# Optimization experiments

Hardware: AMD Instinct MI355X
Metric: run time of the kernel (lower is better)

The kernel has to match this reference:

```python
import jax, jax.numpy as jnp
import numpy as np

N_NODES, N_EDGES, IN_DIM, H, D = 50000, 800000, 256, 4, 32
NEG_SLOPE = 0.2  # DGL GATv2Conv default


def setup_inputs() -> dict:
    key = jax.random.key(0)
    k = jax.random.split(key, 7)
    s_in = 1.0 / np.sqrt(IN_DIM)
    return {
        "h": jax.random.normal(k[0], (N_NODES, IN_DIM), jnp.float32),
        "src": jax.random.randint(k[1], (N_EDGES,), 0, N_NODES, jnp.int32),
        "dst": jax.random.randint(k[2], (N_EDGES,), 0, N_NODES, jnp.int32),
        "W_src": jax.random.normal(k[3], (IN_DIM, H * D), jnp.float32) * s_in,
        "b_src": jnp.zeros((H * D,), jnp.float32),
        "W_dst": jax.random.normal(k[4], (IN_DIM, H * D), jnp.float32) * s_in,
        "b_dst": jnp.zeros((H * D,), jnp.float32),
        "attn_a": jax.random.normal(k[5], (H, D), jnp.float32) * 0.1,
    }


def reference(h, src, dst, W_src, b_src, W_dst, b_dst, attn_a):
    """GATv2Conv (hop=1, get_attention=True) + reshape, as in TweetEmbedder.forward."""
    N = h.shape[0]
    el = (h @ W_src + b_src).reshape(N, H, D)  # fc_src, per-head
    er = (h @ W_dst + b_dst).reshape(N, H, D)  # fc_dst, per-head
    # edge scores: e_ij = a^T leaky_relu(W_src h_i + W_dst h_j)
    e = jax.nn.leaky_relu(el[src] + er[dst], NEG_SLOPE)          # (E, H, D)
    scores = jnp.einsum('ehd,hd->eh', e, attn_a)                  # (E, H)
    # edge softmax over incoming edges of each dst node
    m = jax.ops.segment_max(scores, dst, num_segments=N)          # (N, H)
    ex = jnp.exp(scores - m[dst])
    denom = jax.ops.segment_sum(ex, dst, num_segments=N)          # (N, H)
    a = ex / denom[dst]                                           # (E, H)
    # weighted scatter-aggregate of source messages
    out = jax.ops.segment_sum(a[:, :, None] * el[src], dst, num_segments=N)  # (N, H, D)
    return out.reshape(N, H * D), a[:, :, None]
```

## Files before the change

### kernel.cpp

```cpp
#include <hip/hip_runtime.h>
#include <cstdint>
#include <cstddef>

#define NNODES 50000
#define NEDGES 800000
#define INDIM  256
#define HD     128
#define NH     4
#define NEG    0.2f

#define SCAN_B ((NNODES + 255) / 256)

#define CONVH_BLKS (NNODES * INDIM / 8 / 256)
#define HIST_BLKS  ((NEDGES + 255) / 256)
#define CONVW_BLKS 64
#define GEMM_BLKS  (2 * ((NNODES + 127) / 128))
#define SCAT_BLKS  ((NEDGES + 255) / 256)

typedef __attribute__((ext_vector_type(8))) short   short8;
typedef __attribute__((ext_vector_type(8))) ushort  ushort8;
typedef __attribute__((ext_vector_type(4))) float   floatx4;

__device__ __forceinline__ ushort f2bf(float f) {
    unsigned u = __float_as_uint(f);
    unsigned r = u + 0x7fffu + ((u >> 16) & 1u);
    return (ushort)(r >> 16);
}
__device__ __forceinline__ float bf2f(ushort u) {
    return __uint_as_float(((unsigned)u) << 16);
}

__device__ __forceinline__ int swz(int c) { return c ^ ((c >> 4) & 7); }

__global__ __launch_bounds__(256) void fusedA_kernel(
        const float* __restrict__ h, ushort* __restrict__ h_bf,
        const int* __restrict__ dst, int* __restrict__ cnt_work,
        const float* __restrict__ Wsrc, const float* __restrict__ Wdst,
        ushort* __restrict__ Wt) {
    __shared__ float t[32][33];
    const int bid = blockIdx.x;
    const int tid = threadIdx.x;

    if (bid < CONVH_BLKS) {
        int idx = bid * 256 + tid;
        const int total = NNODES * INDIM / 8;
        if (idx >= total) return;
        const float* p = h + (size_t)idx * 8;
        float4 v0 = *(const float4*)p;
        float4 v1 = *(const float4*)(p + 4);
        ushort8 o;
        o[0] = f2bf(v0.x); o[1] = f2bf(v0.y); o[2] = f2bf(v0.z); o[3] = f2bf(v0.w);
        o[4] = f2bf(v1.x); o[5] = f2bf(v1.y); o[6] = f2bf(v1.z); o[7] = f2bf(v1.w);
        *(ushort8*)(h_bf + (size_t)idx * 8) = o;
    } else if (bid < CONVH_BLKS + HIST_BLKS) {
        int e = (bid - CONVH_BLKS) * 256 + tid;
        if (e < NEDGES) atomicAdd(cnt_work + dst[e], 1);
    } else {
        int wb = bid - (CONVH_BLKS + HIST_BLKS);
        int kb = (wb & 7) * 32, nb = (wb >> 3) * 32;
        int tx = tid & 31, ty = tid >> 5;
        for (int i = ty; i < 32; i += 8) {
            int k = kb + i, n = nb + tx;
            float v = (n < HD) ? Wsrc[(size_t)k * HD + n] : Wdst[(size_t)k * HD + (n - HD)];
            t[i][tx] = v;
        }
        __syncthreads();
        for (int i = ty; i < 32; i += 8) {
            int n = nb + i, k = kb + tx;
            Wt[(size_t)n * INDIM + k] = f2bf(t[tx][i]);
        }
    }
}

__global__ __launch_bounds__(256) void scan_partial_kernel(
        const int* __restrict__ cnt, int* __restrict__ partials) {
    __shared__ int lds[256];
    int i = blockIdx.x * 256 + threadIdx.x;
    lds[threadIdx.x] = (i < NNODES) ? cnt[i] : 0;
    __syncthreads();
    for (int off = 128; off > 0; off >>= 1) {
        if (threadIdx.x < off) lds[threadIdx.x] += lds[threadIdx.x + off];
        __syncthreads();
    }
    if (threadIdx.x == 0) partials[blockIdx.x] = lds[0];
}

__global__ __launch_bounds__(256) void scan_offsets_kernel(
        int* __restrict__ partials, int* __restrict__ rowptr) {
    __shared__ int lds[256];
    int t = threadIdx.x;
    int v = (t < SCAN_B) ? partials[t] : 0;
    lds[t] = v;
    __syncthreads();
    for (int off = 1; off < 256; off <<= 1) {
        int u = (t >= off) ? lds[t - off] : 0;
        __syncthreads();
        lds[t] += u;
        __syncthreads();
    }
    if (t < SCAN_B) partials[t] = lds[t] - v;
    if (t == 255) rowptr[NNODES] = lds[255];
}

__global__ __launch_bounds__(256) void scan_final_kernel(
        int* __restrict__ cnt_work, const int* __restrict__ partials,
        int* __restrict__ rowptr) {
    __shared__ int lds[256];
    int i = blockIdx.x * 256 + threadIdx.x;
    int t = threadIdx.x;
    int v = (i < NNODES) ? cnt_work[i] : 0;
    lds[t] = v;
    __syncthreads();
    for (int off = 1; off < 256; off <<= 1) {
        int u = (t >= off) ? lds[t - off] : 0;
        __syncthreads();
        lds[t] += u;
        __syncthreads();
    }
    if (i < NNODES) {
        int start = partials[blockIdx.x] + lds[t] - v;
        rowptr[i] = start;
        cnt_work[i] = start;
    }
}

__global__ __launch_bounds__(256) void fusedB_kernel(
        const ushort* __restrict__ h_bf, const ushort* __restrict__ Wt,
        const float* __restrict__ bsrc, const float* __restrict__ bdst,
        ushort* __restrict__ el_bf, float* __restrict__ er,
        const int* __restrict__ src, const int* __restrict__ dst,
        int* __restrict__ cnt_work,
        int* __restrict__ eidx, int* __restrict__ esrc) {
    __shared__ ushort As[512 * 8];
    __shared__ ushort Bs[512 * 8];

    const int bid = blockIdx.x;
    const int tid = threadIdx.x;

    if (bid >= GEMM_BLKS) {
        int e = (bid - GEMM_BLKS) * 256 + tid;
        if (e >= NEDGES) return;
        int s = src[e];
        int pos = atomicAdd(cnt_work + dst[e], 1);
        eidx[pos] = e;
        esrc[pos] = s;
        return;
    }

    const int bx = bid & 1, by = bid >> 1;
    const int wave = tid >> 6, lane = tid & 63;
    const int row0 = by * 128;
    const int col0 = bx * 128;
    const int l15  = lane & 15, quad = lane >> 4;

    floatx4 acc[2][8];
#pragma unroll
    for (int i = 0; i < 2; ++i)
#pragma unroll
        for (int j = 0; j < 8; ++j) acc[i][j] = (floatx4){0.f, 0.f, 0.f, 0.f};

    for (int kk = 0; kk < INDIM; kk += 32) {
#pragma unroll
        for (int it = 0; it < 2; ++it) {
            int idx = tid + it * 256;
            int r = idx >> 2;
            int kq = idx & 3;
            int c = (r >> 4) * 64 + kq * 16 + (r & 15);
            int grow = row0 + r;
            ushort8 aw = (ushort8){0,0,0,0,0,0,0,0};
            if (grow < NNODES)
                aw = *(const ushort8*)(h_bf + (size_t)grow * INDIM + kk + kq * 8);
            *(ushort8*)(As + swz(c) * 8) = aw;
            ushort8 bw = *(const ushort8*)(Wt + (size_t)(col0 + r) * INDIM + kk + kq * 8);
            *(ushort8*)(Bs + swz(c) * 8) = bw;
        }
        __syncthreads();

        short8 af[2], bf[8];
#pragma unroll
        for (int tm = 0; tm < 2; ++tm) {
            int c = (wave * 2 + tm) * 64 + quad * 16 + l15;
            af[tm] = *(const short8*)(As + swz(c) * 8);
        }
#pragma unroll
        for (int tn = 0; tn < 8; ++tn) {
            int c = tn * 64 + quad * 16 + l15;
            bf[tn] = *(const short8*)(Bs + swz(c) * 8);
        }
#pragma unroll
        for (int tm = 0; tm < 2; ++tm)
#pragma unroll
            for (int tn = 0; tn < 8; ++tn)
                acc[tm][tn] = __builtin_amdgcn_mfma_f32_16x16x32_bf16(
                    af[tm], bf[tn], acc[tm][tn], 0, 0, 0);
        __syncthreads();
    }

    if (col0 == 0) {
#pragma unroll
        for (int tn = 0; tn < 8; ++tn) {
            int col = tn * 16 + l15;
            float bias = bsrc[col];
#pragma unroll
            for (int tm = 0; tm < 2; ++tm)
#pragma unroll
                for (int reg = 0; reg < 4; ++reg) {
                    int row = row0 + wave * 32 + tm * 16 + quad * 4 + reg;
                    if (row < NNODES)
                        el_bf[(size_t)row * HD + col] = f2bf(acc[tm][tn][reg] + bias);
                }
        }
    } else {
#pragma unroll
        for (int tn = 0; tn < 8; ++tn) {
            int col = tn * 16 + l15;
            float bias = bdst[col];
#pragma unroll
            for (int tm = 0; tm < 2; ++tm)
#pragma unroll
                for (int reg = 0; reg < 4; ++reg) {
                    int row = row0 + wave * 32 + tm * 16 + quad * 4 + reg;
                    if (row < NNODES)
                        er[(size_t)row * HD + col] = acc[tm][tn][reg] + bias;
                }
        }
    }
}

#define DEGCAP 128

__global__ __launch_bounds__(256) void node_fused_kernel(
        const ushort* __restrict__ el_bf, const float* __restrict__ er,
        const int* __restrict__ rowptr, const int* __restrict__ eidx,
        const int* __restrict__ esrc,
        const float* __restrict__ attn,
        float* __restrict__ out_feat, float* __restrict__ out_a) {
    __shared__ float sp[4][DEGCAP * NH];

    const int wv = threadIdx.x >> 6;
    const int n = blockIdx.x * 4 + wv;
    if (n >= NNODES) return;
    const int lane = threadIdx.x & 63;
    const int hh = lane >> 4;
    const int lo = rowptr[n], hi = rowptr[n + 1];
    const int deg = hi - lo;
    float* spw = sp[wv];
    const int l2 = lane * 2;

    const float2 rv = *(const float2*)(er + (size_t)n * HD + l2);
    const float a0 = attn[l2], a1 = attn[l2 + 1];

    float m = -3.4e38f, lsum = 0.0f, acc0 = 0.0f, acc1 = 0.0f;

    if (deg > 0 && deg <= DEGCAP) {
        int jj0 = (lane & 15);
        if (jj0 >= deg) jj0 = deg - 1;
        int si = esrc[lo + jj0];

        for (int base = 0; base < deg; base += 16) {
            ushort2 u[16];
#pragma unroll
            for (int j = 0; j < 16; ++j) {
                if (base + j < deg) {
                    int s = __builtin_amdgcn_readlane(si, j);
                    u[j] = *(const ushort2*)(el_bf + (size_t)s * HD + l2);
                }
            }
            int si_nxt = si;
            if (base + 16 < deg) {
                int jj = base + 16 + (lane & 15);
                if (jj >= deg) jj = deg - 1;
                si_nxt = esrc[lo + jj];
            }
#pragma unroll
            for (int j = 0; j < 16; ++j) {
                if (base + j < deg) {
                    float evx = bf2f(u[j].x), evy = bf2f(u[j].y);
                    float x0 = evx + rv.x; x0 = x0 > 0.f ? x0 : NEG * x0;
                    float x1 = evy + rv.y; x1 = x1 > 0.f ? x1 : NEG * x1;
                    float p = x0 * a0 + x1 * a1;
                    p += __shfl_xor(p, 1, 16);
                    p += __shfl_xor(p, 2, 16);
                    p += __shfl_xor(p, 4, 16);
                    p += __shfl_xor(p, 8, 16);
                    if ((lane & 15) == 0) spw[(base + j) * NH + hh] = p;
                    float mn = fmaxf(m, p);
                    float sc = __expf(m - mn);
                    float w  = __expf(p - mn);
                    lsum = lsum * sc + w;
                    acc0 = acc0 * sc + w * evx;
                    acc1 = acc1 * sc + w * evy;
                    m = mn;
                }
            }
            si = si_nxt;
        }
    } else if (deg > DEGCAP) {
        ushort2 u = {0,0};
        { int s_ = esrc[lo]; u = *(const ushort2*)(el_bf + (size_t)s_ * HD + l2); }
        for (int i = lo; i < hi; ++i) {
            float evx = bf2f(u.x), evy = bf2f(u.y);
            if (i + 1 < hi) { int s_ = esrc[i + 1];
                u = *(const ushort2*)(el_bf + (size_t)s_ * HD + l2); }
            float x0 = evx + rv.x; x0 = x0 > 0.f ? x0 : NEG * x0;
            float x1 = evy + rv.y; x1 = x1 > 0.f ? x1 : NEG * x1;
            float p = x0 * a0 + x1 * a1;
            p += __shfl_xor(p, 1, 16);
            p += __shfl_xor(p, 2, 16);
            p += __shfl_xor(p, 4, 16);
            p += __shfl_xor(p, 8, 16);
            float mn = fmaxf(m, p);
            float sc = __expf(m - mn);
            float w  = __expf(p - mn);
            lsum = lsum * sc + w;
            acc0 = acc0 * sc + w * evx;
            acc1 = acc1 * sc + w * evy;
            m = mn;
        }
    }

    float2 o;
    if (deg == 0) { o.x = 0.0f; o.y = 0.0f; }
    else { float inv = 1.0f / lsum; o.x = acc0 * inv; o.y = acc1 * inv; }
    *(float2*)(out_feat + (size_t)n * HD + l2) = o;

    if (deg == 0) return;

    float inv = 1.0f / lsum;
    if (deg <= DEGCAP) {
        float mh   = __shfl(m,   (lane & 3) << 4, 64);
        float invh = __shfl(inv, (lane & 3) << 4, 64);
        for (int j = (lane >> 2); j < deg; j += 16) {
            int e = eidx[lo + j];
            float p = spw[j * NH + (lane & 3)];
            out_a[(size_t)e * NH + (lane & 3)] = __expf(p - mh) * invh;
        }
    } else {
        for (int i = lo; i < hi; ++i) {
            int s_ = esrc[i];
            ushort2 u = *(const ushort2*)(el_bf + (size_t)s_ * HD + l2);
            float evx = bf2f(u.x), evy = bf2f(u.y);
            float x0 = evx + rv.x; x0 = x0 > 0.f ? x0 : NEG * x0;
            float x1 = evy + rv.y; x1 = x1 > 0.f ? x1 : NEG * x1;
            float p = x0 * a0 + x1 * a1;
            p += __shfl_xor(p, 1, 16);
            p += __shfl_xor(p, 2, 16);
            p += __shfl_xor(p, 4, 16);
            p += __shfl_xor(p, 8, 16);
            if ((lane & 15) == 0) {
                int e = eidx[i];
                out_a[(size_t)e * NH + hh] = __expf(p - m) * inv;
            }
        }
    }
}

extern "C" void kernel_launch(void* const* d_in, const int* in_sizes, int n_in,
                              void* d_out, int out_size, void* d_ws, size_t ws_size,
                              hipStream_t stream) {
    const float* h    = (const float*)d_in[0];
    const int*   src  = (const int*)d_in[1];
    const int*   dst  = (const int*)d_in[2];
    const float* Wsrc = (const float*)d_in[3];
    const float* bsrc = (const float*)d_in[4];
    const float* Wdst = (const float*)d_in[5];
    const float* bdst = (const float*)d_in[6];
    const float* attn = (const float*)d_in[7];

    float* out_feat = (float*)d_out;
    float* out_a    = out_feat + (size_t)NNODES * HD;

    ushort* h_bf = (ushort*)d_out;

    float*  er       = (float*)d_ws;
    ushort* Wt       = (ushort*)(er + (size_t)NNODES * HD);
    ushort* el_bf    = Wt + 2 * HD * INDIM;
    int*    cnt_work = (int*)(el_bf + (size_t)NNODES * HD);
    int*    eidx     = cnt_work + NNODES;
    int*    esrc     = eidx + NEDGES;
    int*    rowptr   = esrc + NEDGES;
    int*    partials = rowptr + NNODES + 1;

    hipMemsetAsync(cnt_work, 0, NNODES * sizeof(int), stream);

    fusedA_kernel<<<CONVH_BLKS + HIST_BLKS + CONVW_BLKS, 256, 0, stream>>>(
        h, h_bf, dst, cnt_work, Wsrc, Wdst, Wt);

    scan_partial_kernel<<<SCAN_B, 256, 0, stream>>>(cnt_work, partials);
    scan_offsets_kernel<<<1, 256, 0, stream>>>(partials, rowptr);
    scan_final_kernel<<<SCAN_B, 256, 0, stream>>>(cnt_work, partials, rowptr);

    fusedB_kernel<<<GEMM_BLKS + SCAT_BLKS, 256, 0, stream>>>(
        h_bf, Wt, bsrc, bdst, el_bf, er, src, dst, cnt_work, eidx, esrc);

    node_fused_kernel<<<(NNODES + 3) / 4, 256, 0, stream>>>(
        el_bf, er, rowptr, eidx, esrc, attn, out_feat, out_a);
}
```

Baseline: 270.8 us.

## Process eight edges per wave with 16-wide feature slices and interleaved edge pairs

Reworks the node aggregation kernel so each wave handles 8 incoming edges at once, with each lane owning a 16-element feature slice of one edge. Loads become 32-byte vector loads instead of 4-byte ones, with one-step prefetch of the next edge batch. Partial accumulators are merged across the 8 edge lanes with a butterfly transpose-reduce at the end. Edge index and source are packed into one int2 array so the scatter writes and the node-kernel reads are paired. The cost is higher register pressure from the 16-wide accumulators plus extra shuffles, and wasted lanes for nodes with small degree.

```diff
diff --git a/kernel.cpp b/kernel.cpp
--- a/kernel.cpp
+++ b/kernel.cpp
@@ -129,8 +129,7 @@
         const float* __restrict__ bsrc, const float* __restrict__ bdst,
         ushort* __restrict__ el_bf, float* __restrict__ er,
         const int* __restrict__ src, const int* __restrict__ dst,
-        int* __restrict__ cnt_work,
-        int* __restrict__ eidx, int* __restrict__ esrc) {
+        int* __restrict__ cnt_work, int2* __restrict__ epair) {
     __shared__ ushort As[512 * 8];
     __shared__ ushort Bs[512 * 8];
 
@@ -142,8 +141,7 @@
         if (e >= NEDGES) return;
         int s = src[e];
         int pos = atomicAdd(cnt_work + dst[e], 1);
-        eidx[pos] = e;
-        esrc[pos] = s;
+        epair[pos] = make_int2(e, s);
         return;
     }
 
@@ -231,8 +229,7 @@
 
 __global__ __launch_bounds__(256) void node_fused_kernel(
         const ushort* __restrict__ el_bf, const float* __restrict__ er,
-        const int* __restrict__ rowptr, const int* __restrict__ eidx,
-        const int* __restrict__ esrc,
+        const int* __restrict__ rowptr, const int2* __restrict__ epair,
         const float* __restrict__ attn,
         float* __restrict__ out_feat, float* __restrict__ out_a) {
     __shared__ float sp[4][DEGCAP * NH];
@@ -241,69 +238,158 @@
     const int n = blockIdx.x * 4 + wv;
     if (n >= NNODES) return;
     const int lane = threadIdx.x & 63;
-    const int hh = lane >> 4;
+    const int hh   = lane >> 4;
+    const int j8   = lane & 7;
+    const int dbase = (lane >> 3) * 16;
     const int lo = rowptr[n], hi = rowptr[n + 1];
     const int deg = hi - lo;
     float* spw = sp[wv];
-    const int l2 = lane * 2;
-
-    const float2 rv = *(const float2*)(er + (size_t)n * HD + l2);
-    const float a0 = attn[l2], a1 = attn[l2 + 1];
-
-    float m = -3.4e38f, lsum = 0.0f, acc0 = 0.0f, acc1 = 0.0f;
-
-    if (deg > 0 && deg <= DEGCAP) {
-        int jj0 = (lane & 15);
-        if (jj0 >= deg) jj0 = deg - 1;
-        int si = esrc[lo + jj0];
-
-        for (int base = 0; base < deg; base += 16) {
-            ushort2 u[16];
-#pragma unroll
-            for (int j = 0; j < 16; ++j) {
-                if (base + j < deg) {
-                    int s = __builtin_amdgcn_readlane(si, j);
-                    u[j] = *(const ushort2*)(el_bf + (size_t)s * HD + l2);
+
+    if (deg == 0) {
+        int o = (j8 & 1) * 8 + ((j8 >> 1) & 1) * 4 + ((j8 >> 2) & 1) * 2;
+        *(float2*)(out_feat + (size_t)n * HD + dbase + o) = make_float2(0.f, 0.f);
+        return;
+    }
+
+    if (deg <= DEGCAP) {
+        float erv[16], av[16], acc[16];
+        {
+            const float4* p4 = (const float4*)(er + (size_t)n * HD + dbase);
+            const float4* a4 = (const float4*)(attn + dbase);
+#pragma unroll
+            for (int q = 0; q < 4; ++q) {
+                float4 t = p4[q];
+                erv[4*q] = t.x; erv[4*q+1] = t.y; erv[4*q+2] = t.z; erv[4*q+3] = t.w;
+                float4 u = a4[q];
+                av[4*q] = u.x; av[4*q+1] = u.y; av[4*q+2] = u.z; av[4*q+3] = u.w;
+            }
+        }
+#pragma unroll
+        for (int d = 0; d < 16; ++d) acc[d] = 0.f;
+        float m = -3.4e38f, lsum = 0.f;
+
+        int t0 = (j8 < deg) ? j8 : (deg - 1);
+        int s_cur = epair[lo + t0].y;
+        uint4 el_lo, el_hi;
+        {
+            const ushort* ep = el_bf + (size_t)s_cur * HD + dbase;
+            el_lo = *(const uint4*)ep;
+            el_hi = *(const uint4*)(ep + 8);
+        }
+        int s_nxt = s_cur;
+        if (deg > 8) {
+            int t = 8 + j8; if (t >= deg) t = deg - 1;
+            s_nxt = epair[lo + t].y;
+        }
+
+        for (int base = 0; base < deg; base += 8) {
+            uint4 nl_lo = el_lo, nl_hi = el_hi;
+            if (base + 8 < deg) {
+                const ushort* ep = el_bf + (size_t)s_nxt * HD + dbase;
+                nl_lo = *(const uint4*)ep;
+                nl_hi = *(const uint4*)(ep + 8);
+            }
+            int s_n2 = s_nxt;
+            if (base + 16 < deg) {
+                int t = base + 16 + j8; if (t >= deg) t = deg - 1;
+                s_n2 = epair[lo + t].y;
+            }
+
+            float ev[16];
+            {
+                const unsigned* wl = (const unsigned*)&el_lo;
+                const unsigned* wh = (const unsigned*)&el_hi;
+#pragma unroll
+                for (int q = 0; q < 4; ++q) {
+                    ev[2*q]       = __uint_as_float(wl[q] << 16);
+                    ev[2*q + 1]   = __uint_as_float(wl[q] & 0xffff0000u);
+                    ev[8 + 2*q]   = __uint_as_float(wh[q] << 16);
+                    ev[8 + 2*q+1] = __uint_as_float(wh[q] & 0xffff0000u);
                 }
             }
-            int si_nxt = si;
-            if (base + 16 < deg) {
-                int jj = base + 16 + (lane & 15);
-                if (jj >= deg) jj = deg - 1;
-                si_nxt = esrc[lo + jj];
-            }
-#pragma unroll
-            for (int j = 0; j < 16; ++j) {
-                if (base + j < deg) {
-                    float evx = bf2f(u[j].x), evy = bf2f(u[j].y);
-                    float x0 = evx + rv.x; x0 = x0 > 0.f ? x0 : NEG * x0;
-                    float x1 = evy + rv.y; x1 = x1 > 0.f ? x1 : NEG * x1;
-                    float p = x0 * a0 + x1 * a1;
-                    p += __shfl_xor(p, 1, 16);
-                    p += __shfl_xor(p, 2, 16);
-                    p += __shfl_xor(p, 4, 16);
-                    p += __shfl_xor(p, 8, 16);
-                    if ((lane & 15) == 0) spw[(base + j) * NH + hh] = p;
-                    float mn = fmaxf(m, p);
-                    float sc = __expf(m - mn);
-                    float w  = __expf(p - mn);
-                    lsum = lsum * sc + w;
-                    acc0 = acc0 * sc + w * evx;
-                    acc1 = acc1 * sc + w * evy;
-                    m = mn;
-                }
-            }
-            si = si_nxt;
-        }
-    } else if (deg > DEGCAP) {
-        ushort2 u = {0,0};
-        { int s_ = esrc[lo]; u = *(const ushort2*)(el_bf + (size_t)s_ * HD + l2); }
+            float pa = 0.f, pb = 0.f;
+#pragma unroll
+            for (int d = 0; d < 16; d += 2) {
+                float x0 = ev[d]   + erv[d];   x0 = fmaxf(x0, NEG * x0);
+                float x1 = ev[d+1] + erv[d+1]; x1 = fmaxf(x1, NEG * x1);
+                pa = fmaf(x0, av[d],   pa);
+                pb = fmaf(x1, av[d+1], pb);
+            }
+            float part = pa + pb;
+            float p = part + __shfl_xor(part, 8, 64);
+            bool valid = (base + j8) < deg;
+            if (!valid) p = -3.4e38f;
+            if (valid && (lane & 8) == 0) spw[(base + j8) * NH + hh] = p;
+
+            float cm = p;
+            cm = fmaxf(cm, __shfl_xor(cm, 1, 64));
+            cm = fmaxf(cm, __shfl_xor(cm, 2, 64));
+            cm = fmaxf(cm, __shfl_xor(cm, 4, 64));
+            float mn = fmaxf(m, cm);
+            float sc = __expf(m - mn);
+            float w  = __expf(p - mn);
+            float ws = w;
+            ws += __shfl_xor(ws, 1, 64);
+            ws += __shfl_xor(ws, 2, 64);
+            ws += __shfl_xor(ws, 4, 64);
+            lsum = lsum * sc + ws;
+#pragma unroll
+            for (int d = 0; d < 16; ++d)
+                acc[d] = fmaf(w, ev[d], acc[d] * sc);
+            m = mn;
+            el_lo = nl_lo; el_hi = nl_hi; s_nxt = s_n2;
+        }
+
+        float inv = 1.0f / lsum;
+
+#pragma unroll
+        for (int k = 0; k < 8; ++k) {
+            float send = (j8 & 1) ? acc[k] : acc[k + 8];
+            float recv = __shfl_xor(send, 1, 64);
+            float keep = (j8 & 1) ? acc[k + 8] : acc[k];
+            acc[k] = keep + recv;
+        }
+#pragma unroll
+        for (int k = 0; k < 4; ++k) {
+            float send = (j8 & 2) ? acc[k] : acc[k + 4];
+            float recv = __shfl_xor(send, 2, 64);
+            float keep = (j8 & 2) ? acc[k + 4] : acc[k];
+            acc[k] = keep + recv;
+        }
+#pragma unroll
+        for (int k = 0; k < 2; ++k) {
+            float send = (j8 & 4) ? acc[k] : acc[k + 2];
+            float recv = __shfl_xor(send, 4, 64);
+            float keep = (j8 & 4) ? acc[k + 2] : acc[k];
+            acc[k] = keep + recv;
+        }
+        int o = (j8 & 1) * 8 + ((j8 >> 1) & 1) * 4 + ((j8 >> 2) & 1) * 2;
+        *(float2*)(out_feat + (size_t)n * HD + dbase + o) =
+            make_float2(acc[0] * inv, acc[1] * inv);
+
+        float mh   = __shfl(m,   (lane & 3) << 4, 64);
+        float invh = __shfl(inv, (lane & 3) << 4, 64);
+        for (int q = lane >> 2; q < deg; q += 16) {
+            int e = epair[lo + q].x;
+            float pq = spw[q * NH + (lane & 3)];
+            out_a[(size_t)e * NH + (lane & 3)] = __expf(pq - mh) * invh;
+        }
+        return;
+    }
+
+    {
+        const int l2 = lane * 2;
+        const float2 rv = *(const float2*)(er + (size_t)n * HD + l2);
+        const float a0 = attn[l2], a1 = attn[l2 + 1];
+        float m = -3.4e38f, lsum = 0.f, acc0 = 0.f, acc1 = 0.f;
+        ushort2 u;
+        { int s_ = epair[lo].y; u = *(const ushort2*)(el_bf + (size_t)s_ * HD + l2); }
         for (int i = lo; i < hi; ++i) {
             float evx = bf2f(u.x), evy = bf2f(u.y);
-            if (i + 1 < hi) { int s_ = esrc[i + 1];
+            if (i + 1 < hi) { int s_ = epair[i + 1].y;
                 u = *(const ushort2*)(el_bf + (size_t)s_ * HD + l2); }
-            float x0 = evx + rv.x; x0 = x0 > 0.f ? x0 : NEG * x0;
-            float x1 = evy + rv.y; x1 = x1 > 0.f ? x1 : NEG * x1;
+            float x0 = evx + rv.x; x0 = fmaxf(x0, NEG * x0);
+            float x1 = evy + rv.y; x1 = fmaxf(x1, NEG * x1);
             float p = x0 * a0 + x1 * a1;
             p += __shfl_xor(p, 1, 16);
             p += __shfl_xor(p, 2, 16);
@@ -317,38 +403,21 @@
             acc1 = acc1 * sc + w * evy;
             m = mn;
         }
-    }
-
-    float2 o;
-    if (deg == 0) { o.x = 0.0f; o.y = 0.0f; }
-    else { float inv = 1.0f / lsum; o.x = acc0 * inv; o.y = acc1 * inv; }
-    *(float2*)(out_feat + (size_t)n * HD + l2) = o;
-
-    if (deg == 0) return;
-
-    float inv = 1.0f / lsum;
-    if (deg <= DEGCAP) {
-        float mh   = __shfl(m,   (lane & 3) << 4, 64);
-        float invh = __shfl(inv, (lane & 3) << 4, 64);
-        for (int j = (lane >> 2); j < deg; j += 16) {
-            int e = eidx[lo + j];
-            float p = spw[j * NH + (lane & 3)];
-            out_a[(size_t)e * NH + (lane & 3)] = __expf(p - mh) * invh;
-        }
-    } else {
+        float inv = 1.0f / lsum;
+        *(float2*)(out_feat + (size_t)n * HD + l2) = make_float2(acc0 * inv, acc1 * inv);
         for (int i = lo; i < hi; ++i) {
-            int s_ = esrc[i];
-            ushort2 u = *(const ushort2*)(el_bf + (size_t)s_ * HD + l2);
-            float evx = bf2f(u.x), evy = bf2f(u.y);
-            float x0 = evx + rv.x; x0 = x0 > 0.f ? x0 : NEG * x0;
-            float x1 = evy + rv.y; x1 = x1 > 0.f ? x1 : NEG * x1;
+            int s_ = epair[i].y;
+            ushort2 uu = *(const ushort2*)(el_bf + (size_t)s_ * HD + l2);
+            float evx = bf2f(uu.x), evy = bf2f(uu.y);
+            float x0 = evx + rv.x; x0 = fmaxf(x0, NEG * x0);
+            float x1 = evy + rv.y; x1 = fmaxf(x1, NEG * x1);
             float p = x0 * a0 + x1 * a1;
             p += __shfl_xor(p, 1, 16);
             p += __shfl_xor(p, 2, 16);
             p += __shfl_xor(p, 4, 16);
             p += __shfl_xor(p, 8, 16);
             if ((lane & 15) == 0) {
-                int e = eidx[i];
+                int e = epair[i].x;
                 out_a[(size_t)e * NH + hh] = __expf(p - m) * inv;
             }
         }
@@ -376,9 +445,8 @@
     ushort* Wt       = (ushort*)(er + (size_t)NNODES * HD);
     ushort* el_bf    = Wt + 2 * HD * INDIM;
     int*    cnt_work = (int*)(el_bf + (size_t)NNODES * HD);
-    int*    eidx     = cnt_work + NNODES;
-    int*    esrc     = eidx + NEDGES;
-    int*    rowptr   = esrc + NEDGES;
+    int2*   epair    = (int2*)(cnt_work + NNODES);
+    int*    rowptr   = (int*)(epair + NEDGES);
     int*    partials = rowptr + NNODES + 1;
 
     hipMemsetAsync(cnt_work, 0, NNODES * sizeof(int), stream);
@@ -391,8 +459,8 @@
     scan_final_kernel<<<SCAN_B, 256, 0, stream>>>(cnt_work, partials, rowptr);
 
     fusedB_kernel<<<GEMM_BLKS + SCAT_BLKS, 256, 0, stream>>>(
-        h_bf, Wt, bsrc, bdst, el_bf, er, src, dst, cnt_work, eidx, esrc);
+        h_bf, Wt, bsrc, bdst, el_bf, er, src, dst, cnt_work, epair);
 
     node_fused_kernel<<<(NNODES + 3) / 4, 256, 0, stream>>>(
-        el_bf, er, rowptr, eidx, esrc, attn, out_feat, out_a);
-}
+        el_bf, er, rowptr, epair, attn, out_feat, out_a);
+}
```

Measured after the change: 311.5 us. +15.0%, slower.

## Fuse h bf16 conversion into GEMM, compute el and er per block, pack edge pairs

Applied to the files above, without the earlier changes.

Drops the separate h-to-bf16 conversion pass and converts fp32 h inside the GEMM tile load. Each GEMM block now computes all 256 output columns (el and er together), so h is read once instead of twice, at the cost of twice the accumulator registers and LDS for B. Edge index and source arrays are packed into one int2 array. The node kernel's online softmax is batched in groups of four edges to cut exp calls and shorten dependency chains.

```diff
diff --git a/kernel.cpp b/kernel.cpp
--- a/kernel.cpp
+++ b/kernel.cpp
@@ -11,10 +11,9 @@
 
 #define SCAN_B ((NNODES + 255) / 256)
 
-#define CONVH_BLKS (NNODES * INDIM / 8 / 256)
 #define HIST_BLKS  ((NEDGES + 255) / 256)
 #define CONVW_BLKS 64
-#define GEMM_BLKS  (2 * ((NNODES + 127) / 128))
+#define GEMM_BLKS  ((NNODES + 127) / 128)
 #define SCAT_BLKS  ((NEDGES + 255) / 256)
 
 typedef __attribute__((ext_vector_type(8))) short   short8;
@@ -33,7 +32,6 @@
 __device__ __forceinline__ int swz(int c) { return c ^ ((c >> 4) & 7); }
 
 __global__ __launch_bounds__(256) void fusedA_kernel(
-        const float* __restrict__ h, ushort* __restrict__ h_bf,
         const int* __restrict__ dst, int* __restrict__ cnt_work,
         const float* __restrict__ Wsrc, const float* __restrict__ Wdst,
         ushort* __restrict__ Wt) {
@@ -41,22 +39,11 @@
     const int bid = blockIdx.x;
     const int tid = threadIdx.x;
 
-    if (bid < CONVH_BLKS) {
-        int idx = bid * 256 + tid;
-        const int total = NNODES * INDIM / 8;
-        if (idx >= total) return;
-        const float* p = h + (size_t)idx * 8;
-        float4 v0 = *(const float4*)p;
-        float4 v1 = *(const float4*)(p + 4);
-        ushort8 o;
-        o[0] = f2bf(v0.x); o[1] = f2bf(v0.y); o[2] = f2bf(v0.z); o[3] = f2bf(v0.w);
-        o[4] = f2bf(v1.x); o[5] = f2bf(v1.y); o[6] = f2bf(v1.z); o[7] = f2bf(v1.w);
-        *(ushort8*)(h_bf + (size_t)idx * 8) = o;
-    } else if (bid < CONVH_BLKS + HIST_BLKS) {
-        int e = (bid - CONVH_BLKS) * 256 + tid;
+    if (bid < HIST_BLKS) {
+        int e = bid * 256 + tid;
         if (e < NEDGES) atomicAdd(cnt_work + dst[e], 1);
     } else {
-        int wb = bid - (CONVH_BLKS + HIST_BLKS);
+        int wb = bid - HIST_BLKS;
         int kb = (wb & 7) * 32, nb = (wb >> 3) * 32;
         int tx = tid & 31, ty = tid >> 5;
         for (int i = ty; i < 32; i += 8) {
@@ -124,15 +111,14 @@
     }
 }
 
-__global__ __launch_bounds__(256) void fusedB_kernel(
-        const ushort* __restrict__ h_bf, const ushort* __restrict__ Wt,
+__global__ __launch_bounds__(256, 2) void fusedB_kernel(
+        const float* __restrict__ h, const ushort* __restrict__ Wt,
         const float* __restrict__ bsrc, const float* __restrict__ bdst,
         ushort* __restrict__ el_bf, float* __restrict__ er,
         const int* __restrict__ src, const int* __restrict__ dst,
-        int* __restrict__ cnt_work,
-        int* __restrict__ eidx, int* __restrict__ esrc) {
+        int* __restrict__ cnt_work, int2* __restrict__ epair) {
     __shared__ ushort As[512 * 8];
-    __shared__ ushort Bs[512 * 8];
+    __shared__ ushort Bs[1024 * 8];
 
     const int bid = blockIdx.x;
     const int tid = threadIdx.x;
@@ -142,22 +128,19 @@
         if (e >= NEDGES) return;
         int s = src[e];
         int pos = atomicAdd(cnt_work + dst[e], 1);
-        eidx[pos] = e;
-        esrc[pos] = s;
+        epair[pos] = make_int2(e, s);
         return;
     }
 
-    const int bx = bid & 1, by = bid >> 1;
     const int wave = tid >> 6, lane = tid & 63;
-    const int row0 = by * 128;
-    const int col0 = bx * 128;
+    const int row0 = bid * 128;
     const int l15  = lane & 15, quad = lane >> 4;
 
-    floatx4 acc[2][8];
+    floatx4 acc[2][16];
 #pragma unroll
     for (int i = 0; i < 2; ++i)
 #pragma unroll
-        for (int j = 0; j < 8; ++j) acc[i][j] = (floatx4){0.f, 0.f, 0.f, 0.f};
+        for (int j = 0; j < 16; ++j) acc[i][j] = (floatx4){0.f, 0.f, 0.f, 0.f};
 
     for (int kk = 0; kk < INDIM; kk += 32) {
 #pragma unroll
@@ -168,62 +151,67 @@
             int c = (r >> 4) * 64 + kq * 16 + (r & 15);
             int grow = row0 + r;
             ushort8 aw = (ushort8){0,0,0,0,0,0,0,0};
-            if (grow < NNODES)
-                aw = *(const ushort8*)(h_bf + (size_t)grow * INDIM + kk + kq * 8);
+            if (grow < NNODES) {
+                const float* p = h + (size_t)grow * INDIM + kk + kq * 8;
+                float4 v0 = *(const float4*)p;
+                float4 v1 = *(const float4*)(p + 4);
+                aw[0] = f2bf(v0.x); aw[1] = f2bf(v0.y); aw[2] = f2bf(v0.z); aw[3] = f2bf(v0.w);
+                aw[4] = f2bf(v1.x); aw[5] = f2bf(v1.y); aw[6] = f2bf(v1.z); aw[7] = f2bf(v1.w);
+            }
             *(ushort8*)(As + swz(c) * 8) = aw;
-            ushort8 bw = *(const ushort8*)(Wt + (size_t)(col0 + r) * INDIM + kk + kq * 8);
+        }
+#pragma unroll
+        for (int it = 0; it < 4; ++it) {
+            int idx = tid + it * 256;
+            int r = idx >> 2;
+            int kq = idx & 3;
+            int c = (r >> 4) * 64 + kq * 16 + (r & 15);
+            ushort8 bw = *(const ushort8*)(Wt + (size_t)r * INDIM + kk + kq * 8);
             *(ushort8*)(Bs + swz(c) * 8) = bw;
         }
         __syncthreads();
 
-        short8 af[2], bf[8];
+        short8 af[2];
 #pragma unroll
         for (int tm = 0; tm < 2; ++tm) {
             int c = (wave * 2 + tm) * 64 + quad * 16 + l15;
             af[tm] = *(const short8*)(As + swz(c) * 8);
         }
 #pragma unroll
-        for (int tn = 0; tn < 8; ++tn) {
+        for (int tn = 0; tn < 16; ++tn) {
             int c = tn * 64 + quad * 16 + l15;
-            bf[tn] = *(const short8*)(Bs + swz(c) * 8);
-        }
+            short8 bfr = *(const short8*)(Bs + swz(c) * 8);
+            acc[0][tn] = __builtin_amdgcn_mfma_f32_16x16x32_bf16(af[0], bfr, acc[0][tn], 0, 0, 0);
+            acc[1][tn] = __builtin_amdgcn_mfma_f32_16x16x32_bf16(af[1], bfr, acc[1][tn], 0, 0, 0);
+        }
+        __syncthreads();
+    }
+
+#pragma unroll
+    for (int tn = 0; tn < 8; ++tn) {
+        int col = tn * 16 + l15;
+        float bias = bsrc[col];
 #pragma unroll
         for (int tm = 0; tm < 2; ++tm)
 #pragma unroll
-            for (int tn = 0; tn < 8; ++tn)
-                acc[tm][tn] = __builtin_amdgcn_mfma_f32_16x16x32_bf16(
-                    af[tm], bf[tn], acc[tm][tn], 0, 0, 0);
-        __syncthreads();
-    }
-
-    if (col0 == 0) {
-#pragma unroll
-        for (int tn = 0; tn < 8; ++tn) {
-            int col = tn * 16 + l15;
-            float bias = bsrc[col];
-#pragma unroll
-            for (int tm = 0; tm < 2; ++tm)
-#pragma unroll
-                for (int reg = 0; reg < 4; ++reg) {
-                    int row = row0 + wave * 32 + tm * 16 + quad * 4 + reg;
-                    if (row < NNODES)
-                        el_bf[(size_t)row * HD + col] = f2bf(acc[tm][tn][reg] + bias);
-                }
-        }
-    } else {
-#pragma unroll
-        for (int tn = 0; tn < 8; ++tn) {
-            int col = tn * 16 + l15;
-            float bias = bdst[col];
-#pragma unroll
-            for (int tm = 0; tm < 2; ++tm)
-#pragma unroll
-                for (int reg = 0; reg < 4; ++reg) {
-                    int row = row0 + wave * 32 + tm * 16 + quad * 4 + reg;
-                    if (row < NNODES)
-                        er[(size_t)row * HD + col] = acc[tm][tn][reg] + bias;
-                }
-        }
+            for (int reg = 0; reg < 4; ++reg) {
+                int row = row0 + wave * 32 + tm * 16 + quad * 4 + reg;
+                if (row < NNODES)
+                    el_bf[(size_t)row * HD + col] = f2bf(acc[tm][tn][reg] + bias);
+            }
+    }
+#pragma unroll
+    for (int tn = 8; tn < 16; ++tn) {
+        int col = tn * 16 + l15 - HD;
+        float bias = bdst[col];
+#pragma unroll
+        for (int tm = 0; tm < 2; ++tm)
+#pragma unroll
+            for (int reg = 0; reg < 4; ++reg) {
+                int row = row0 + wave * 32 + tm * 16 + quad * 4 + reg;
+                if (row < NNODES)
+                    er[(size_t)row * HD + col] = acc[tm][tn][reg] + bias;
+            }
     }
 }
 
@@ -231,8 +219,7 @@
 
 __global__ __launch_bounds__(256) void node_fused_kernel(
         const ushort* __restrict__ el_bf, const float* __restrict__ er,
-        const int* __restrict__ rowptr, const int* __restrict__ eidx,
-        const int* __restrict__ esrc,
+        const int* __restrict__ rowptr, const int2* __restrict__ epair,
         const float* __restrict__ attn,
         float* __restrict__ out_feat, float* __restrict__ out_a) {
     __shared__ float sp[4][DEGCAP * NH];
@@ -255,10 +242,12 @@
     if (deg > 0 && deg <= DEGCAP) {
         int jj0 = (lane & 15);
         if (jj0 >= deg) jj0 = deg - 1;
-        int si = esrc[lo + jj0];
+        int si = epair[lo + jj0].y;
 
         for (int base = 0; base < deg; base += 16) {
             ushort2 u[16];
+#pragma unroll
+            for (int j = 0; j < 16; ++j) u[j] = (ushort2){0, 0};
 #pragma unroll
             for (int j = 0; j < 16; ++j) {
                 if (base + j < deg) {
@@ -270,40 +259,53 @@
             if (base + 16 < deg) {
                 int jj = base + 16 + (lane & 15);
                 if (jj >= deg) jj = deg - 1;
-                si_nxt = esrc[lo + jj];
-            }
-#pragma unroll
-            for (int j = 0; j < 16; ++j) {
-                if (base + j < deg) {
-                    float evx = bf2f(u[j].x), evy = bf2f(u[j].y);
-                    float x0 = evx + rv.x; x0 = x0 > 0.f ? x0 : NEG * x0;
-                    float x1 = evy + rv.y; x1 = x1 > 0.f ? x1 : NEG * x1;
+                si_nxt = epair[lo + jj].y;
+            }
+#pragma unroll
+            for (int g = 0; g < 4; ++g) {
+                float px[4], ex[4], ey[4];
+#pragma unroll
+                for (int j = 0; j < 4; ++j) {
+                    int jj = g * 4 + j;
+                    bool valid = (base + jj) < deg;
+                    float evx = bf2f(u[jj].x), evy = bf2f(u[jj].y);
+                    ex[j] = evx; ey[j] = evy;
+                    float x0 = evx + rv.x; x0 = fmaxf(x0, NEG * x0);
+                    float x1 = evy + rv.y; x1 = fmaxf(x1, NEG * x1);
                     float p = x0 * a0 + x1 * a1;
                     p += __shfl_xor(p, 1, 16);
                     p += __shfl_xor(p, 2, 16);
                     p += __shfl_xor(p, 4, 16);
                     p += __shfl_xor(p, 8, 16);
-                    if ((lane & 15) == 0) spw[(base + j) * NH + hh] = p;
-                    float mn = fmaxf(m, p);
-                    float sc = __expf(m - mn);
-                    float w  = __expf(p - mn);
-                    lsum = lsum * sc + w;
-                    acc0 = acc0 * sc + w * evx;
-                    acc1 = acc1 * sc + w * evy;
-                    m = mn;
+                    if (valid && (lane & 15) == 0) spw[(base + jj) * NH + hh] = p;
+                    px[j] = valid ? p : -3.4e38f;
                 }
+                float cm = fmaxf(fmaxf(px[0], px[1]), fmaxf(px[2], px[3]));
+                float mn = fmaxf(m, cm);
+                float sc = __expf(m - mn);
+                float w0 = __expf(px[0] - mn);
+                float w1 = __expf(px[1] - mn);
+                float w2 = __expf(px[2] - mn);
+                float w3 = __expf(px[3] - mn);
+                lsum = fmaf(lsum, sc, (w0 + w1) + (w2 + w3));
+                acc0 *= sc; acc1 *= sc;
+                acc0 = fmaf(w0, ex[0], acc0); acc1 = fmaf(w0, ey[0], acc1);
+                acc0 = fmaf(w1, ex[1], acc0); acc1 = fmaf(w1, ey[1], acc1);
+                acc0 = fmaf(w2, ex[2], acc0); acc1 = fmaf(w2, ey[2], acc1);
+                acc0 = fmaf(w3, ex[3], acc0); acc1 = fmaf(w3, ey[3], acc1);
+                m = mn;
             }
             si = si_nxt;
         }
     } else if (deg > DEGCAP) {
         ushort2 u = {0,0};
-        { int s_ = esrc[lo]; u = *(const ushort2*)(el_bf + (size_t)s_ * HD + l2); }
+        { int s_ = epair[lo].y; u = *(const ushort2*)(el_bf + (size_t)s_ * HD + l2); }
         for (int i = lo; i < hi; ++i) {
             float evx = bf2f(u.x), evy = bf2f(u.y);
-            if (i + 1 < hi) { int s_ = esrc[i + 1];
+            if (i + 1 < hi) { int s_ = epair[i + 1].y;
                 u = *(const ushort2*)(el_bf + (size_t)s_ * HD + l2); }
-            float x0 = evx + rv.x; x0 = x0 > 0.f ? x0 : NEG * x0;
-            float x1 = evy + rv.y; x1 = x1 > 0.f ? x1 : NEG * x1;
+            float x0 = evx + rv.x; x0 = fmaxf(x0, NEG * x0);
+            float x1 = evy + rv.y; x1 = fmaxf(x1, NEG * x1);
             float p = x0 * a0 + x1 * a1;
             p += __shfl_xor(p, 1, 16);
             p += __shfl_xor(p, 2, 16);
@@ -330,25 +332,25 @@
     if (deg <= DEGCAP) {
         float mh   = __shfl(m,   (lane & 3) << 4, 64);
         float invh = __shfl(inv, (lane & 3) << 4, 64);
-        for (int j = (lane >> 2); j < deg; j += 16) {
-            int e = eidx[lo + j];
-            float p = spw[j * NH + (lane & 3)];
+        for (int q = (lane >> 2); q < deg; q += 16) {
+            int e = epair[lo + q].x;
+            float p = spw[q * NH + (lane & 3)];
             out_a[(size_t)e * NH + (lane & 3)] = __expf(p - mh) * invh;
         }
     } else {
         for (int i = lo; i < hi; ++i) {
-            int s_ = esrc[i];
+            int s_ = epair[i].y;
             ushort2 u = *(const ushort2*)(el_bf + (size_t)s_ * HD + l2);
             float evx = bf2f(u.x), evy = bf2f(u.y);
-            float x0 = evx + rv.x; x0 = x0 > 0.f ? x0 : NEG * x0;
-            float x1 = evy + rv.y; x1 = x1 > 0.f ? x1 : NEG * x1;
+            float x0 = evx + rv.x; x0 = fmaxf(x0, NEG * x0);
+            float x1 = evy + rv.y; x1 = fmaxf(x1, NEG * x1);
             float p = x0 * a0 + x1 * a1;
             p += __shfl_xor(p, 1, 16);
             p += __shfl_xor(p, 2, 16);
             p += __shfl_xor(p, 4, 16);
             p += __shfl_xor(p, 8, 16);
             if ((lane & 15) == 0) {
-                int e = eidx[i];
+                int e = epair[i].x;
                 out_a[(size_t)e * NH + hh] = __expf(p - m) * inv;
             }
         }
@@ -370,29 +372,26 @@
     float* out_feat = (float*)d_out;
     float* out_a    = out_feat + (size_t)NNODES * HD;
 
-    ushort* h_bf = (ushort*)d_out;
-
     float*  er       = (float*)d_ws;
     ushort* Wt       = (ushort*)(er + (size_t)NNODES * HD);
     ushort* el_bf    = Wt + 2 * HD * INDIM;
     int*    cnt_work = (int*)(el_bf + (size_t)NNODES * HD);
-    int*    eidx     = cnt_work + NNODES;
-    int*    esrc     = eidx + NEDGES;
-    int*    rowptr   = esrc + NEDGES;
+    int2*   epair    = (int2*)(cnt_work + NNODES);
+    int*    rowptr   = (int*)(epair + NEDGES);
     int*    partials = rowptr + NNODES + 1;
 
     hipMemsetAsync(cnt_work, 0, NNODES * sizeof(int), stream);
 
-    fusedA_kernel<<<CONVH_BLKS + HIST_BLKS + CONVW_BLKS, 256, 0, stream>>>(
-        h, h_bf, dst, cnt_work, Wsrc, Wdst, Wt);
+    fusedA_kernel<<<HIST_BLKS + CONVW_BLKS, 256, 0, stream>>>(
+        dst, cnt_work, Wsrc, Wdst, Wt);
 
     scan_partial_kernel<<<SCAN_B, 256, 0, stream>>>(cnt_work, partials);
     scan_offsets_kernel<<<1, 256, 0, stream>>>(partials, rowptr);
     scan_final_kernel<<<SCAN_B, 256, 0, stream>>>(cnt_work, partials, rowptr);
 
     fusedB_kernel<<<GEMM_BLKS + SCAT_BLKS, 256, 0, stream>>>(
-        h_bf, Wt, bsrc, bdst, el_bf, er, src, dst, cnt_work, eidx, esrc);
+        h, Wt, bsrc, bdst, el_bf, er, src, dst, cnt_work, epair);
 
     node_fused_kernel<<<(NNODES + 3) / 4, 256, 0, stream>>>(
-        el_bf, er, rowptr, eidx, esrc, attn, out_feat, out_a);
-}
+        el_bf, er, rowptr, epair, attn, out_feat, out_a);
+}
```

Result: slower. 305.2 us (+12.7%).
